# Performance work log

Measured on AMD Instinct MI355X. Metric: run time of the kernel, lower is better.

The kernel has to match this reference:

```python
import jax, jax.numpy as jnp
import numpy as np

A = 3                      # anchors per location
HS = [256, 128, 64, 32]    # square feature-map sizes (FPN levels)
B = 4                      # batch (num images)
SIZES = [A * h * h for h in HS]
T = sum(SIZES)             # 261120 anchors per image
PRE_N, POST_N = 512, 512
NMS_TH, SCORE_TH, MIN_SIZE = 0.7, 0.0, 1e-3
LOG_MAX = 4.135166556742356   # log(1000/16), standard delta clamp
MAXV = 8                      # max vertices of quad-quad intersection
LVL_OFF = 8192.0              # per-level coordinate offset for batched NMS


def box_corners(b):
    # b: [..., 5] (cx, cy, w, h, angle) -> [..., 4, 2] CCW corners
    cx, cy, w, h, a = (b[..., i] for i in range(5))
    c, s = jnp.cos(a), jnp.sin(a)
    dx = 0.5 * jnp.stack([w, -w, -w, w], -1)
    dy = 0.5 * jnp.stack([h, h, -h, -h], -1)
    x = cx[..., None] + dx * c[..., None] - dy * s[..., None]
    y = cy[..., None] + dx * s[..., None] + dy * c[..., None]
    return jnp.stack([x, y], -1)


def _clip(poly, cnt, p1, p2):
    # Sutherland-Hodgman clip of poly (padded [MAXV,2], cnt valid) by half-plane left of p1->p2
    e = p2 - p1
    d = e[0] * (poly[:, 1] - p1[1]) - e[1] * (poly[:, 0] - p1[0])
    def body(carry, i):
        out, oc = carry
        nxt = jnp.where(i + 1 < cnt, i + 1, 0)
        cur_in, nxt_in = d[i] >= 0, d[nxt] >= 0
        valid = i < cnt
        keep = valid & cur_in
        out = out.at[oc].set(jnp.where(keep, poly[i], out[oc]))
        oc = oc + keep.astype(jnp.int32)
        crs = valid & (cur_in != nxt_in)
        den = d[i] - d[nxt]
        t = d[i] / jnp.where(den == 0, 1.0, den)
        ip = poly[i] + t * (poly[nxt] - poly[i])
        out = out.at[oc].set(jnp.where(crs, ip, out[oc]))
        oc = oc + crs.astype(jnp.int32)
        return (out, oc), None
    (out, oc), _ = jax.lax.scan(body, (jnp.zeros((MAXV, 2), poly.dtype), jnp.int32(0)), jnp.arange(MAXV))
    return out, oc


def _inter_area(ca, cb):
    # intersection area of two convex quads given CCW corners [4,2]
    poly = jnp.zeros((MAXV, 2), ca.dtype).at[:4].set(ca)
    cnt = jnp.int32(4)
    for k in range(4):
        poly, cnt = _clip(poly, cnt, cb[k], cb[(k + 1) % 4])
    i = jnp.arange(MAXV)
    nxt = jnp.where(i + 1 < cnt, i + 1, 0)
    cr = poly[i, 0] * poly[nxt, 1] - poly[nxt, 0] * poly[i, 1]
    area = 0.5 * jnp.abs(jnp.sum(jnp.where(i < cnt, cr, 0.0)))
    return jnp.where(cnt >= 3, area, 0.0)


def decode(deltas, anchors):
    # XYWHA decode with 6-dim deltas (dx,dy,dw,dh,dsin,dcos), weights all 1.0
    ax, ay, aw, ah, aa = (anchors[..., i] for i in range(5))
    dx, dy, dw, dh, ds, dc = (deltas[..., i] for i in range(6))
    dw = jnp.minimum(dw, LOG_MAX)
    dh = jnp.minimum(dh, LOG_MAX)
    return jnp.stack([ax + dx * aw, ay + dy * ah, aw * jnp.exp(dw),
                      ah * jnp.exp(dh), aa + jnp.arctan2(ds, dc)], -1)


def nms_image(boxes, scores, levels):
    # boxes [N,5], scores [N] (post-sigmoid), levels [N] int32 -> fixed-size padded outputs
    N = scores.shape[0]
    valid = (boxes[:, 2] >= MIN_SIZE) & (boxes[:, 3] >= MIN_SIZE) & (scores >= SCORE_TH)
    s = jnp.where(valid, scores, -jnp.inf)
    order = jnp.argsort(-s)
    bx, sc, vd = boxes[order], s[order], valid[order]
    off = levels[order].astype(bx.dtype) * LVL_OFF
    nb = bx.at[:, :2].add(off[:, None])          # level offset => cross-level IoU == 0
    nbg = jax.lax.stop_gradient(nb)
    corners = box_corners(nbg)                    # [N,4,2]
    areas = nbg[:, 2] * nbg[:, 3]
    CH = 128
    def chunk_fn(args):
        cc, ca = args
        def row(ci, ai):
            inter = jax.vmap(lambda cj: _inter_area(ci, cj))(corners)
            return inter / (ai + areas - inter + 1e-7)
        return jax.vmap(row)(cc, ca)
    iou = jax.lax.map(chunk_fn, (corners.reshape(N // CH, CH, 4, 2),
                                 areas.reshape(N // CH, CH))).reshape(N, N)
    idx = jnp.arange(N)
    def body(i, sup):
        keep_i = ~sup[i]
        return sup | (keep_i & (iou[i] > NMS_TH) & (idx > i))
    sup = jax.lax.fori_loop(0, N, body, ~vd)      # invalid boxes start suppressed
    kept = ~sup
    _, top_i = jax.lax.top_k(jnp.where(kept, sc, -jnp.inf), POST_N)
    ok = kept[top_i]
    return jnp.where(ok[:, None], bx[top_i], 0.0), jnp.where(ok, sc[top_i], 0.0)


def rpn_forward(objs, dlts, anchors):
    obj_f, dlt_f = [], []
    for o, d, h in zip(objs, dlts, HS):
        # permute_and_flatten: [B,A,H,W] -> [B,H*W*A]; [B,A*6,H,W] -> [B,H*W*A,6]
        obj_f.append(o.transpose(0, 2, 3, 1).reshape(B, -1))
        dlt_f.append(d.reshape(B, A, 6, h, h).transpose(0, 3, 4, 1, 2).reshape(B, -1, 6))
    objectness = jnp.concatenate(obj_f, 1)        # [B, T]
    deltas = jnp.concatenate(dlt_f, 1)            # [B, T, 6]
    proposals = decode(deltas, anchors)           # [B, T, 5]
    parts, offset = [], 0
    for sz in SIZES:                               # per-level top-k
        k = min(PRE_N, sz)
        _, ti = jax.lax.top_k(objectness[:, offset:offset + sz], k)
        parts.append(ti + offset)
        offset += sz
    top_idx = jnp.concatenate(parts, 1)           # [B, 4*PRE_N]
    levels = jnp.concatenate([jnp.full((sz,), i, jnp.int32) for i, sz in enumerate(SIZES)])
    obj_top = jnp.take_along_axis(objectness, top_idx, 1)
    prop_top = jnp.take_along_axis(proposals, top_idx[..., None], 1)
    lvl_top = levels[top_idx]
    scores = jax.nn.sigmoid(obj_top)
    return jax.vmap(nms_image)(prop_top, scores, lvl_top)


def setup_inputs() -> dict:
    key = jax.random.key(0)
    ks = jax.random.split(key, 9)
    inp = {}
    for i, h in enumerate(HS):
        inp[f"obj{i}"] = jax.random.normal(ks[i], (B, A, h, h), jnp.float32)
        inp[f"dlt{i}"] = 0.25 * jax.random.normal(ks[4 + i], (B, A * 6, h, h), jnp.float32)
    u = jax.random.uniform(ks[8], (B, T, 5), jnp.float32)
    inp["anchors"] = jnp.stack([u[..., 0] * 1024.0, u[..., 1] * 1024.0,
                                8.0 + 120.0 * u[..., 2], 8.0 + 120.0 * u[..., 3],
                                jnp.pi * (u[..., 4] - 0.5)], -1)
    return inp


def reference(obj0, obj1, obj2, obj3, dlt0, dlt1, dlt2, dlt3, anchors):
    # returns (boxes [B, POST_N, 5], scores [B, POST_N]) padded with zeros
    return rpn_forward([obj0, obj1, obj2, obj3], [dlt0, dlt1, dlt2, dlt3], anchors)
```

## Files before the change

kernel.cpp:

```cpp
#include <hip/hip_runtime.h>

typedef unsigned int u32;
typedef unsigned long long u64;
typedef unsigned char u8;

#define NB 4
#define T_ANCH 261120
#define NCAND 2048
#define KSEL 512
#define POSTN 512
#define LOG_MAXF 4.135166556742356f
#define NMS_TH 0.7f
#define LVL_OFF_F 8192.0f
#define BINS 4096
#define EQCAP 8192
#define K5_BLOCKS 2048
#define K1_BLOCKS 256

__device__ __forceinline__ u32 mono32(float f){
  u32 u = __float_as_uint(f);
  return (u & 0x80000000u) ? ~u : (u | 0x80000000u);
}
__device__ __forceinline__ int lvl_hw(int lvl){ return 65536 >> (2*lvl); }
__device__ __forceinline__ int lvl_off(int lvl){
  return (lvl>0?196608:0) + (lvl>1?49152:0) + (lvl>2?12288:0);
}
__device__ __forceinline__ void k1_map(int bx, int& b, int& lvl, int& ch){
  b = bx >> 6;
  int c = bx & 63;
  if (c < 48){ lvl = 0; ch = c; }
  else if (c < 60){ lvl = 1; ch = c - 48; }
  else if (c < 63){ lvl = 2; ch = c - 60; }
  else { lvl = 3; ch = 0; }
}

__global__ __launch_bounds__(1024) void k1_hist_thresh(
    const float* __restrict__ o0, const float* __restrict__ o1,
    const float* __restrict__ o2, const float* __restrict__ o3,
    u32* __restrict__ hist16, u32* __restrict__ done16,
    u32* __restrict__ gb0, u32* __restrict__ gcA)
{
  int b, lvl, ch;
  k1_map(blockIdx.x, b, lvl, ch);
  int bid16 = b*4 + lvl;
  int nch = (lvl==0?48 : lvl==1?12 : lvl==2?3 : 1);
  const float* ob = (lvl==0)?o0 : (lvl==1)?o1 : (lvl==2)?o2 : o3;
  int hw = lvl_hw(lvl);
  int size = 3*hw;
  int n4 = size >> 2;
  int i4 = ch*1024 + threadIdx.x;
  __shared__ u32 hist[BINS];
  __shared__ u32 coarse[64];
  __shared__ int s_last;
  for (int i = threadIdx.x; i < BINS; i += 1024) hist[i] = 0;
  __syncthreads();
  if (i4 < n4){
    float4 v = ((const float4*)(ob + (size_t)b*size))[i4];
    atomicAdd(&hist[mono32(v.x) >> 20], 1u);
    atomicAdd(&hist[mono32(v.y) >> 20], 1u);
    atomicAdd(&hist[mono32(v.z) >> 20], 1u);
    atomicAdd(&hist[mono32(v.w) >> 20], 1u);
  }
  __syncthreads();
  u32* gh = hist16 + (size_t)bid16*BINS;
  for (int i = threadIdx.x; i < BINS; i += 1024){
    u32 c = hist[i];
    if (c) atomicAdd(&gh[i], c);
  }
  __syncthreads();
  if (threadIdx.x == 0){
    __threadfence();
    u32 d = atomicAdd(&done16[bid16], 1u);
    s_last = (d == (u32)(nch - 1)) ? 1 : 0;
  }
  __syncthreads();
  if (!s_last) return;

  __threadfence();
  for (int i = threadIdx.x; i < BINS; i += 1024)
    hist[i] = __hip_atomic_load(&gh[i], __ATOMIC_RELAXED, __HIP_MEMORY_SCOPE_AGENT);
  __syncthreads();
  int t = threadIdx.x;
  if (t < 64){
    u32 s = 0;
    for (int z = 0; z < 64; ++z) s += hist[t*64 + z];
    coarse[t] = s;
  }
  __syncthreads();
  if (t == 0){
    u32 acc = 0;
    int cb = 63;
    while (acc + coarse[cb] < (u32)KSEL){ acc += coarse[cb]; --cb; }
    int z = cb*64 + 63;
    while (acc + hist[z] < (u32)KSEL){ acc += hist[z]; --z; }
    gb0[bid16] = (u32)z;
    gcA[bid16] = acc;
  }
}

__global__ __launch_bounds__(1024) void k2_classify(
    const float* __restrict__ o0, const float* __restrict__ o1,
    const float* __restrict__ o2, const float* __restrict__ o3,
    const u32* __restrict__ gb0,
    u32* __restrict__ emitcnt, u32* __restrict__ tiecnt,
    int* __restrict__ cand_j, u64* __restrict__ gtie)
{
  int b, lvl, ch;
  k1_map(blockIdx.x, b, lvl, ch);
  int bid16 = b*4 + lvl;
  const float* ob = (lvl==0)?o0 : (lvl==1)?o1 : (lvl==2)?o2 : o3;
  int hw = lvl_hw(lvl);
  int size = 3*hw;
  int n4 = size >> 2;
  int i4 = ch*1024 + threadIdx.x;

  __shared__ u32 dbuf[KSEL];
  __shared__ u64 tbuf[4096];
  __shared__ u32 dn, tn, dbase, tbase;
  if (threadIdx.x == 0){ dn = 0; tn = 0; }
  __syncthreads();

  u32 b0v = gb0[bid16];
  if (i4 < n4){
    float4 v = ((const float4*)(ob + (size_t)b*size))[i4];
    int L = i4 << 2;
    int a = L / hw;
    int pix = L - a*hw;
    int j0 = pix*3 + a;
    float vv[4] = {v.x, v.y, v.z, v.w};
    #pragma unroll
    for (int q = 0; q < 4; ++q){
      u32 m = mono32(vv[q]);
      u32 bin = m >> 20;
      int j = j0 + 3*q;
      if (bin > b0v){
        u32 s = atomicAdd(&dn, 1u);
        if (s < (u32)KSEL) dbuf[s] = (u32)j;
      } else if (bin == b0v){
        u32 s = atomicAdd(&tn, 1u);
        if (s < 4096u) tbuf[s] = ((u64)m << 32) | (u32)(~(u32)j);
      }
    }
  }
  __syncthreads();
  if (threadIdx.x == 0){
    dbase = dn ? atomicAdd(&emitcnt[bid16], dn) : 0u;
    tbase = tn ? atomicAdd(&tiecnt[bid16], tn) : 0u;
  }
  __syncthreads();
  for (u32 x = threadIdx.x; x < dn; x += 1024){
    u32 s = dbase + x;
    if (s < (u32)KSEL) cand_j[bid16*KSEL + s] = (int)dbuf[x];
  }
  for (u32 x = threadIdx.x; x < tn; x += 1024){
    u32 s = tbase + x;
    if (s < (u32)EQCAP) gtie[(size_t)bid16*EQCAP + s] = tbuf[x];
  }
}

__global__ __launch_bounds__(512) void k3_tie_decode(
    const u64* __restrict__ gtie, const u32* __restrict__ tiecnt,
    const u32* __restrict__ gcA, const int* __restrict__ cand_j,
    const float* __restrict__ o0, const float* __restrict__ o1,
    const float* __restrict__ o2, const float* __restrict__ o3,
    const float* __restrict__ d0, const float* __restrict__ d1,
    const float* __restrict__ d2, const float* __restrict__ d3,
    const float* __restrict__ anchors,
    float* __restrict__ cscore, u32* __restrict__ csmono,
    u64* __restrict__ ctb, float* __restrict__ cbox, u8* __restrict__ cvalid)
{
  int bid = blockIdx.x;
  int t = threadIdx.x;
  __shared__ u64 eq[EQCAP];
  __shared__ u32 wbuf[KSEL];
  __shared__ int jlist[KSEL];
  __shared__ u32 wn;
  u32 n = tiecnt[bid]; if (n > (u32)EQCAP) n = (u32)EQCAP;
  u32 cA = gcA[bid];
  u32 k = (u32)KSEL - cA;
  if (t == 0) wn = 0;
  for (int i = t; i < KSEL; i += 512) jlist[i] = 0;
  for (u32 i = t; i < n; i += 512) eq[i] = gtie[(size_t)bid*EQCAP + i];
  __syncthreads();
  for (u32 i = t; i < n; i += 512){
    u64 ki = eq[i];
    u32 r = 0;
    for (u32 m = 0; m < n; ++m) r += (eq[m] > ki) ? 1u : 0u;
    if (r < k){
      u32 s = atomicAdd(&wn, 1u);
      if (s < (u32)KSEL) wbuf[s] = (u32)(~(u32)ki);
    }
  }
  __syncthreads();
  u32 w = wn;
  for (u32 i = t; i < cA; i += 512)
    if (i < (u32)KSEL) jlist[i] = cand_j[bid*KSEL + i];
  for (u32 x = t; x < w; x += 512){
    u32 s = cA + x;
    if (s < (u32)KSEL) jlist[s] = (int)wbuf[x];
  }
  __syncthreads();

  {
    int c = bid*KSEL + t;
    int b = bid >> 2, lvl = bid & 3;
    int j = jlist[t];
    int hw = lvl_hw(lvl);
    u32 pix = (u32)j / 3u;
    u32 a = (u32)j - pix*3u;
    const float* ob = (lvl==0)?o0 : (lvl==1)?o1 : (lvl==2)?o2 : o3;
    const float* dl = (lvl==0)?d0 : (lvl==1)?d1 : (lvl==2)?d2 : d3;

    float ov = ob[(size_t)(b*3 + (int)a)*hw + pix];
    size_t dbase = ((size_t)(b*3 + (int)a)*6)*(size_t)hw + pix;
    float dx  = dl[dbase + 0*(size_t)hw];
    float dy  = dl[dbase + 1*(size_t)hw];
    float dw  = dl[dbase + 2*(size_t)hw];
    float dh  = dl[dbase + 3*(size_t)hw];
    float dsn = dl[dbase + 4*(size_t)hw];
    float dcs = dl[dbase + 5*(size_t)hw];
    int tt = lvl_off(lvl) + j;
    const float* an = anchors + ((size_t)b*T_ANCH + tt)*5;
    float ax=an[0], ay=an[1], aw=an[2], ah=an[3], aa=an[4];
    dw = fminf(dw, LOG_MAXF); dh = fminf(dh, LOG_MAXF);
    float cx = ax + dx*aw;
    float cy = ay + dy*ah;
    float ww = aw * expf(dw);
    float hh = ah * expf(dh);
    float ang = aa + atan2f(dsn, dcs);
    double sd = 1.0 / (1.0 + exp(-(double)ov));
    float sc = (float)sd;
    bool valid = (ww >= 1e-3f) && (hh >= 1e-3f) && (sc >= 0.0f);
    cscore[c] = sc;
    csmono[c] = valid ? mono32(sc) : 0u;
    ctb[c] = ((u64)lvl << 50) | ((u64)(u32)(~mono32(ov)) << 18) | (u64)(u32)j;
    cvalid[c] = valid ? 1 : 0;
    float* bb = cbox + (size_t)c*5;
    bb[0]=cx; bb[1]=cy; bb[2]=ww; bb[3]=hh; bb[4]=ang;
  }
}

__global__ __launch_bounds__(256) void k4_rank(
    const u32* __restrict__ csmono, const u64* __restrict__ ctb,
    const float* __restrict__ cscore, const float* __restrict__ cbox,
    const u8* __restrict__ cvalid,
    float* __restrict__ sscore, float* __restrict__ sbox,
    float* __restrict__ geom, float4* __restrict__ aabb4,
    u8* __restrict__ svalid, u64* __restrict__ maskz, u64* __restrict__ rowflagz)
{
  int b   = blockIdx.x >> 6;
  int blk = blockIdx.x & 63;
  __shared__ u32 sm[NCAND];
  __shared__ u64 stb[NCAND];
  __shared__ u32 cnt[32][8];
  {
    u64* mz = maskz + (size_t)blockIdx.x * 1024;
    for (int x = threadIdx.x; x < 1024; x += 256) mz[x] = 0ull;
    if (threadIdx.x == 0 && blockIdx.x < NB*32) rowflagz[blockIdx.x] = 0ull;
  }
  for (int k = threadIdx.x; k < NCAND; k += 256){
    sm[k]  = csmono[b*NCAND + k];
    stb[k] = ctb[b*NCAND + k];
  }
  __syncthreads();
  int esub = threadIdx.x >> 3;
  int ssub = threadIdx.x & 7;
  int id = blk*32 + esub;
  u32 ms = sm[id];
  u64 mt = stb[id];
  u32 r = 0;
  #pragma unroll 8
  for (int it = 0; it < 256; ++it){
    int m = it*8 + ssub;
    u32 s2 = sm[m]; u64 t2 = stb[m];
    r += ((s2 > ms) || (s2 == ms && t2 < mt)) ? 1u : 0u;
  }
  cnt[esub][ssub] = r;
  __syncthreads();
  if (ssub == 0){
    u32 rank = 0;
    #pragma unroll
    for (int q = 0; q < 8; ++q) rank += cnt[esub][q];
    int gsrc = b*NCAND + id;
    int gdst = b*NCAND + (int)rank;
    sscore[gdst] = cscore[gsrc];
    svalid[gdst] = cvalid[gsrc];
    float b0 = cbox[(size_t)gsrc*5+0], b1 = cbox[(size_t)gsrc*5+1];
    float b2 = cbox[(size_t)gsrc*5+2], b3 = cbox[(size_t)gsrc*5+3];
    float b4 = cbox[(size_t)gsrc*5+4];
    float* sb = sbox + (size_t)gdst*5;
    sb[0]=b0; sb[1]=b1; sb[2]=b2; sb[3]=b3; sb[4]=b4;
    int lvl = (int)((mt >> 50) & 3ull);
    float offv = (float)lvl * LVL_OFF_F;
    float cx = b0 + offv, cy = b1 + offv, w=b2, h=b3, ang=b4;
    float cc = cosf(ang), sn = sinf(ang);
    float hx = 0.5f*w, hy = 0.5f*h;
    float x0 = cx + hx*cc - hy*sn, y0 = cy + hx*sn + hy*cc;
    float x1 = cx - hx*cc - hy*sn, y1 = cy - hx*sn + hy*cc;
    float x2 = cx - hx*cc + hy*sn, y2 = cy - hx*sn - hy*cc;
    float x3 = cx + hx*cc + hy*sn, y3 = cy + hx*sn - hy*cc;
    float minx = fminf(fminf(x0,x1),fminf(x2,x3));
    float maxx = fmaxf(fmaxf(x0,x1),fmaxf(x2,x3));
    float miny = fminf(fminf(y0,y1),fminf(y2,y3));
    float maxy = fmaxf(fmaxf(y0,y1),fmaxf(y2,y3));
    float* g = geom + (size_t)gdst*16;
    g[0]=minx; g[1]=maxx; g[2]=miny; g[3]=maxy; g[4]=w*h;
    g[5]=x0; g[6]=y0; g[7]=x1; g[8]=y1; g[9]=x2; g[10]=y2; g[11]=x3; g[12]=y3;
    aabb4[gdst] = make_float4(minx, maxx, miny, maxy);
  }
}

__device__ __forceinline__ void emit_pt(float* ox, float* oy, int oc, float x, float y){
  #pragma unroll
  for (int s = 0; s < 8; ++s) if (s == oc){ ox[s] = x; oy[s] = y; }
}

__device__ float quad_inter(const float* ca, const float* cb){
  float px[8], py[8];
  #pragma unroll
  for (int q = 0; q < 8; ++q){ px[q]=0.f; py[q]=0.f; }
  #pragma unroll
  for (int q = 0; q < 4; ++q){ px[q]=ca[2*q]; py[q]=ca[2*q+1]; }
  int cnt = 4;
  #pragma unroll
  for (int e = 0; e < 4; ++e){
    float p1x = cb[2*e],         p1y = cb[2*e+1];
    float p2x = cb[(2*e+2)&7],   p2y = cb[(2*e+3)&7];
    float ex = p2x-p1x, ey = p2y-p1y;
    float d[8];
    #pragma unroll
    for (int q = 0; q < 8; ++q) d[q] = ex*(py[q]-p1y) - ey*(px[q]-p1x);
    float ox[8], oy[8];
    #pragma unroll
    for (int q = 0; q < 8; ++q){ ox[q]=0.f; oy[q]=0.f; }
    int oc = 0;
    #pragma unroll
    for (int q = 0; q < 8; ++q){
      if (q < cnt){
        bool last = (q+1 >= cnt);
        float dn  = last ? d[0]  : d[(q+1)&7];
        bool in0 = (d[q] >= 0.0f), in1 = (dn >= 0.0f);
        if (in0){ emit_pt(ox,oy,oc,px[q],py[q]); oc++; }
        if (in0 != in1){
          float pnx = last ? px[0] : px[(q+1)&7];
          float pny = last ? py[0] : py[(q+1)&7];
          float den = d[q] - dn;
          float t = d[q] / ((den == 0.0f) ? 1.0f : den);
          emit_pt(ox,oy,oc, px[q] + t*(pnx-px[q]), py[q] + t*(pny-py[q]));
          oc++;
        }
      }
    }
    cnt = (oc > 8) ? 8 : oc;
    #pragma unroll
    for (int q = 0; q < 8; ++q){ px[q]=ox[q]; py[q]=oy[q]; }
  }
  if (cnt < 3) return 0.0f;
  float s = 0.0f;
  #pragma unroll
  for (int q = 0; q < 8; ++q){
    if (q < cnt){
      bool last = (q+1 >= cnt);
      float pnx = last ? px[0] : px[(q+1)&7];
      float pny = last ? py[0] : py[(q+1)&7];
      s += px[q]*pny - pnx*py[q];
    }
  }
  return 0.5f*fabsf(s);
}

__global__ __launch_bounds__(256) void k5_pairs(
    const float4* __restrict__ aabb4, const float* __restrict__ geom,
    u64* __restrict__ mask, u64* __restrict__ rowflag)
{
  __shared__ u32 lbuf[4096];
  __shared__ u32 lcnt;
  if (threadIdx.x == 0) lcnt = 0;
  __syncthreads();
  int img = blockIdx.x >> 9;
  int kk  = blockIdx.x & 511;
  int lane = threadIdx.x & 63;
  int rows[4] = {2*kk, 2*kk + 1, 2046 - 2*kk, 2047 - 2*kk};
  #pragma unroll
  for (int r = 0; r < 4; ++r){
    int i = rows[r];
    float4 gi = aabb4[img*NCAND + i];
    for (int j = i + 1 + (int)threadIdx.x; j < NCAND; j += 256){
      float4 gj = aabb4[img*NCAND + j];
      bool pass = !(gi.x > gj.y || gj.x > gi.y || gi.z > gj.w || gj.z > gi.w);
      u64 bm = __ballot(pass);
      if (bm){
        int leader = __ffsll((long long)bm) - 1;
        u32 base = 0;
        if (lane == leader) base = atomicAdd(&lcnt, (u32)__popcll(bm));
        base = (u32)__shfl((int)base, leader);
        if (pass){
          u32 off = (u32)__popcll(bm & ((1ull << lane) - 1ull));
          lbuf[base + off] = (u32)((i << 11) | j);
        }
      }
    }
  }
  __syncthreads();
  u32 n = lcnt;
  for (u32 x = threadIdx.x; x < n; x += 256){
    u32 gt = lbuf[x];
    int i = (int)(gt >> 11);
    int j = (int)(gt & (NCAND-1));
    const float* gi = geom + ((size_t)(img*NCAND + i))*16;
    const float* gj = geom + ((size_t)(img*NCAND + j))*16;
    float inter = quad_inter(gi+5, gj+5);
    float iou = inter / (gi[4] + gj[4] - inter + 1e-7f);
    if (iou > NMS_TH){
      atomicOr(&mask[((size_t)(img*NCAND + i))*32 + (j >> 6)], 1ull << (j & 63));
      atomicOr(&rowflag[(size_t)img*32 + (i >> 6)], 1ull << (i & 63));
    }
  }
}

__global__ __launch_bounds__(1024) void k6_nms_out(
    const u64* __restrict__ mask, const u64* __restrict__ rowflag,
    const u8* __restrict__ svalid,
    const float* __restrict__ sbox, const float* __restrict__ sscore,
    float* __restrict__ out)
{
  int b = blockIdx.x;
  __shared__ u32 fid[NCAND];
  __shared__ u32 wcnt[32], wpref[32];
  __shared__ u64 s_kept[32];
  __shared__ u32 pref[32];
  __shared__ u32 s_F;
  int t = threadIdx.x;
  int wid = t >> 6, lane = t & 63;

  if (t < 32) wcnt[t] = (u32)__popcll(rowflag[b*32 + t]);
  __syncthreads();
  if (t == 0){
    u32 run = 0;
    for (int w = 0; w < 32; ++w){ wpref[w] = run; run += wcnt[w]; }
    s_F = run;
  }
  __syncthreads();
  if (t < 32){
    u64 fw = rowflag[b*32 + t];
    u32 o = wpref[t];
    while (fw){
      int bpos = __builtin_ctzll(fw);
      fid[o++] = (u32)(t*64 + bpos);
      fw &= fw - 1;
    }
  }
  for (int x = t; x < POSTN*5; x += 1024) out[(size_t)b*POSTN*5 + x] = 0.0f;
  for (int x = t; x < POSTN;   x += 1024) out[(size_t)NB*POSTN*5 + b*POSTN + x] = 0.0f;
  __syncthreads();

  if (wid == 0){
    u32 slo = 0, shi = 0;
    {
      int wl = lane & 31;
      u64 w = 0;
      for (int q = 0; q < 64; ++q)
        if (!svalid[b*NCAND + wl*64 + q]) w |= (1ull << q);
      slo = (u32)w; shi = (u32)(w >> 32);
    }
    u32 F = s_F;
    const u64* mb = mask + ((size_t)b*NCAND)*32;
    for (u32 f = 0; f < F; f += 8){
      u32 myfid = 0;
      if (f + (lane & 7) < F) myfid = fid[f + (lane & 7)];
      u64 v[8];
      #pragma unroll
      for (int q = 0; q < 8; ++q){
        if (f + q < F){
          u32 fq = (u32)__builtin_amdgcn_readlane((int)myfid, q);
          v[q] = mb[(size_t)fq*32 + (lane & 31)];
        } else v[q] = 0ull;
      }
      #pragma unroll
      for (int q = 0; q < 8; ++q){
        if (f + q < F){
          u32 i = (u32)__builtin_amdgcn_readlane((int)myfid, q);
          int wi = (int)(i >> 6);
          u32 wlo = (u32)__builtin_amdgcn_readlane((int)slo, wi);
          u32 whi = (u32)__builtin_amdgcn_readlane((int)shi, wi);
          u64 w = ((u64)whi << 32) | wlo;
          u32 keep = (u32)((~w >> (i & 63)) & 1ull);
          u64 vm = v[q] & (0ull - (u64)keep);
          slo |= (u32)vm; shi |= (u32)(vm >> 32);
        }
      }
    }
    if (lane < 32) s_kept[lane] = ~(((u64)shi << 32) | slo);
  }
  __syncthreads();

  if (t < 32) pref[t] = (u32)__popcll(s_kept[t]);
  __syncthreads();
  if (t == 0){
    u32 run = 0;
    for (int w = 0; w < 32; ++w){ u32 tv = pref[w]; pref[w] = run; run += tv; }
  }
  __syncthreads();
  for (int i = t; i < NCAND; i += 1024){
    u64 kw = s_kept[i >> 6];
    if ((kw >> (i & 63)) & 1ull){
      u32 rank = pref[i >> 6] + (u32)__popcll(kw & ((1ull << (i & 63)) - 1ull));
      if (rank < POSTN){
        const float* bp = sbox + ((size_t)(b*NCAND + i))*5;
        float* op = out + ((size_t)(b*POSTN + rank))*5;
        op[0]=bp[0]; op[1]=bp[1]; op[2]=bp[2]; op[3]=bp[3]; op[4]=bp[4];
        out[(size_t)NB*POSTN*5 + b*POSTN + rank] = sscore[b*NCAND + i];
      }
    }
  }
}

extern "C" void kernel_launch(void* const* d_in, const int* in_sizes, int n_in,
                              void* d_out, int out_size, void* d_ws, size_t ws_size,
                              hipStream_t stream)
{
  (void)out_size; (void)ws_size;
  const float *obj[4] = {nullptr,nullptr,nullptr,nullptr};
  const float *dlt[4] = {nullptr,nullptr,nullptr,nullptr};
  const float *anchors = nullptr;
  for (int i = 0; i < n_in; ++i){
    int s = in_sizes[i];
    const float* p = (const float*)d_in[i];
    switch (s){
      case 786432:  obj[0] = p; break;
      case 4718592: dlt[0] = p; break;
      case 196608:  obj[1] = p; break;
      case 1179648: dlt[1] = p; break;
      case 49152:   obj[2] = p; break;
      case 294912:  dlt[2] = p; break;
      case 12288:   obj[3] = p; break;
      case 73728:   dlt[3] = p; break;
      case 5222400: anchors = p; break;
      default: break;
    }
  }

  char* wsb = (char*)d_ws;
  size_t off = 0;
  auto alloc = [&](size_t bytes)->void*{
    size_t cur = (off + 255) & ~(size_t)255;
    off = cur + bytes;
    return (void*)(wsb + cur);
  };
  int*   cand_j = (int*)  alloc(16*KSEL*sizeof(int));
  float* cscore = (float*)alloc((size_t)NB*NCAND*sizeof(float));
  u32*   csmono = (u32*)  alloc((size_t)NB*NCAND*sizeof(u32));
  u64*   ctb    = (u64*)  alloc((size_t)NB*NCAND*sizeof(u64));
  float* cbox   = (float*)alloc((size_t)NB*NCAND*5*sizeof(float));
  u8*    cvalid = (u8*)   alloc((size_t)NB*NCAND);
  float* sscore = (float*)alloc((size_t)NB*NCAND*sizeof(float));
  float* sbox   = (float*)alloc((size_t)NB*NCAND*5*sizeof(float));
  u8*    svalid = (u8*)   alloc((size_t)NB*NCAND);
  float* geom   = (float*)alloc((size_t)NB*NCAND*16*sizeof(float));
  float4* aabb4 = (float4*)alloc((size_t)NB*NCAND*sizeof(float4));
  u64*   gtie   = (u64*)  alloc((size_t)16*EQCAP*sizeof(u64));
  u64*   maskp  = (u64*)  alloc((size_t)NB*NCAND*32*sizeof(u64));
  u64*   rowflag= (u64*)  alloc((size_t)NB*32*sizeof(u64));
  u32*   gb0    = (u32*)  alloc(16*sizeof(u32));
  u32*   gcA    = (u32*)  alloc(16*sizeof(u32));
  u32*   hist16 = (u32*)  alloc((size_t)16*BINS*sizeof(u32));
  u32*   done16 = (u32*)  alloc(16*sizeof(u32));
  u32*   emitc  = (u32*)  alloc(16*sizeof(u32));
  u32*   tiec   = (u32*)  alloc(16*sizeof(u32));
  size_t zero_len = (size_t)((wsb + off) - (char*)hist16);

  hipMemsetAsync(hist16, 0, zero_len, stream);

  hipLaunchKernelGGL(k1_hist_thresh, dim3(K1_BLOCKS), dim3(1024), 0, stream,
                     obj[0], obj[1], obj[2], obj[3], hist16, done16, gb0, gcA);
  hipLaunchKernelGGL(k2_classify, dim3(K1_BLOCKS), dim3(1024), 0, stream,
                     obj[0], obj[1], obj[2], obj[3], gb0, emitc, tiec,
                     cand_j, gtie);
  hipLaunchKernelGGL(k3_tie_decode, dim3(16), dim3(512), 0, stream,
                     gtie, tiec, gcA, cand_j,
                     obj[0], obj[1], obj[2], obj[3],
                     dlt[0], dlt[1], dlt[2], dlt[3],
                     anchors, cscore, csmono, ctb, cbox, cvalid);
  hipLaunchKernelGGL(k4_rank, dim3(256), dim3(256), 0, stream,
                     csmono, ctb, cscore, cbox, cvalid, sscore, sbox, geom,
                     aabb4, svalid, maskp, rowflag);
  hipLaunchKernelGGL(k5_pairs, dim3(K5_BLOCKS), dim3(256), 0, stream,
                     aabb4, geom, maskp, rowflag);
  hipLaunchKernelGGL(k6_nms_out, dim3(4), dim3(1024), 0, stream,
                     maskp, rowflag, svalid, sbox, sscore, (float*)d_out);
}
```

Before: 192.3 us.

## Fuse top-k kernels and pair/NMS-output kernels using grid-wide completion counters

Merges the histogram-threshold, classify and tie-decode kernels into one launch. Non-last blocks spin-wait on a published flag for the per-level threshold, and the last block to finish classification does the tie resolution and decode. Likewise, the pair-overlap kernel and the final NMS/output kernel are fused, so the last block per image runs the greedy suppression. This removes launch gaps and the re-read of objectness. The spin-wait relies on all 256 blocks of 1024 threads being co-resident, and the serial tail runs on only one block per group.

```diff
diff --git a/kernel.cpp b/kernel.cpp
--- a/kernel.cpp
+++ b/kernel.cpp
@@ -34,183 +34,191 @@
   else { lvl = 3; ch = 0; }
 }
 
-__global__ __launch_bounds__(1024) void k1_hist_thresh(
-    const float* __restrict__ o0, const float* __restrict__ o1,
-    const float* __restrict__ o2, const float* __restrict__ o3,
-    u32* __restrict__ hist16, u32* __restrict__ done16,
-    u32* __restrict__ gb0, u32* __restrict__ gcA)
-{
-  int b, lvl, ch;
-  k1_map(blockIdx.x, b, lvl, ch);
-  int bid16 = b*4 + lvl;
-  int nch = (lvl==0?48 : lvl==1?12 : lvl==2?3 : 1);
-  const float* ob = (lvl==0)?o0 : (lvl==1)?o1 : (lvl==2)?o2 : o3;
-  int hw = lvl_hw(lvl);
-  int size = 3*hw;
-  int n4 = size >> 2;
-  int i4 = ch*1024 + threadIdx.x;
-  __shared__ u32 hist[BINS];
-  __shared__ u32 coarse[64];
-  __shared__ int s_last;
-  for (int i = threadIdx.x; i < BINS; i += 1024) hist[i] = 0;
-  __syncthreads();
-  if (i4 < n4){
-    float4 v = ((const float4*)(ob + (size_t)b*size))[i4];
-    atomicAdd(&hist[mono32(v.x) >> 20], 1u);
-    atomicAdd(&hist[mono32(v.y) >> 20], 1u);
-    atomicAdd(&hist[mono32(v.z) >> 20], 1u);
-    atomicAdd(&hist[mono32(v.w) >> 20], 1u);
-  }
-  __syncthreads();
-  u32* gh = hist16 + (size_t)bid16*BINS;
-  for (int i = threadIdx.x; i < BINS; i += 1024){
-    u32 c = hist[i];
-    if (c) atomicAdd(&gh[i], c);
-  }
-  __syncthreads();
-  if (threadIdx.x == 0){
-    __threadfence();
-    u32 d = atomicAdd(&done16[bid16], 1u);
-    s_last = (d == (u32)(nch - 1)) ? 1 : 0;
-  }
-  __syncthreads();
-  if (!s_last) return;
-
-  __threadfence();
-  for (int i = threadIdx.x; i < BINS; i += 1024)
-    hist[i] = __hip_atomic_load(&gh[i], __ATOMIC_RELAXED, __HIP_MEMORY_SCOPE_AGENT);
-  __syncthreads();
-  int t = threadIdx.x;
-  if (t < 64){
-    u32 s = 0;
-    for (int z = 0; z < 64; ++z) s += hist[t*64 + z];
-    coarse[t] = s;
-  }
-  __syncthreads();
-  if (t == 0){
-    u32 acc = 0;
-    int cb = 63;
-    while (acc + coarse[cb] < (u32)KSEL){ acc += coarse[cb]; --cb; }
-    int z = cb*64 + 63;
-    while (acc + hist[z] < (u32)KSEL){ acc += hist[z]; --z; }
-    gb0[bid16] = (u32)z;
-    gcA[bid16] = acc;
-  }
-}
-
-__global__ __launch_bounds__(1024) void k2_classify(
-    const float* __restrict__ o0, const float* __restrict__ o1,
-    const float* __restrict__ o2, const float* __restrict__ o3,
-    const u32* __restrict__ gb0,
-    u32* __restrict__ emitcnt, u32* __restrict__ tiecnt,
-    int* __restrict__ cand_j, u64* __restrict__ gtie)
-{
-  int b, lvl, ch;
-  k1_map(blockIdx.x, b, lvl, ch);
-  int bid16 = b*4 + lvl;
-  const float* ob = (lvl==0)?o0 : (lvl==1)?o1 : (lvl==2)?o2 : o3;
-  int hw = lvl_hw(lvl);
-  int size = 3*hw;
-  int n4 = size >> 2;
-  int i4 = ch*1024 + threadIdx.x;
-
-  __shared__ u32 dbuf[KSEL];
-  __shared__ u64 tbuf[4096];
-  __shared__ u32 dn, tn, dbase, tbase;
-  if (threadIdx.x == 0){ dn = 0; tn = 0; }
-  __syncthreads();
-
-  u32 b0v = gb0[bid16];
-  if (i4 < n4){
-    float4 v = ((const float4*)(ob + (size_t)b*size))[i4];
-    int L = i4 << 2;
-    int a = L / hw;
-    int pix = L - a*hw;
-    int j0 = pix*3 + a;
-    float vv[4] = {v.x, v.y, v.z, v.w};
-    #pragma unroll
-    for (int q = 0; q < 4; ++q){
-      u32 m = mono32(vv[q]);
-      u32 bin = m >> 20;
-      int j = j0 + 3*q;
-      if (bin > b0v){
-        u32 s = atomicAdd(&dn, 1u);
-        if (s < (u32)KSEL) dbuf[s] = (u32)j;
-      } else if (bin == b0v){
-        u32 s = atomicAdd(&tn, 1u);
-        if (s < 4096u) tbuf[s] = ((u64)m << 32) | (u32)(~(u32)j);
-      }
-    }
-  }
-  __syncthreads();
-  if (threadIdx.x == 0){
-    dbase = dn ? atomicAdd(&emitcnt[bid16], dn) : 0u;
-    tbase = tn ? atomicAdd(&tiecnt[bid16], tn) : 0u;
-  }
-  __syncthreads();
-  for (u32 x = threadIdx.x; x < dn; x += 1024){
-    u32 s = dbase + x;
-    if (s < (u32)KSEL) cand_j[bid16*KSEL + s] = (int)dbuf[x];
-  }
-  for (u32 x = threadIdx.x; x < tn; x += 1024){
-    u32 s = tbase + x;
-    if (s < (u32)EQCAP) gtie[(size_t)bid16*EQCAP + s] = tbuf[x];
-  }
-}
-
-__global__ __launch_bounds__(512) void k3_tie_decode(
-    const u64* __restrict__ gtie, const u32* __restrict__ tiecnt,
-    const u32* __restrict__ gcA, const int* __restrict__ cand_j,
+union ShA {
+  struct { u32 hist[BINS]; u32 coarse[64]; } a;
+  struct { u32 dbuf[KSEL]; u64 tbuf[4096]; } c;
+  struct { u64 eq[EQCAP]; u32 wbuf[KSEL]; int jlist[KSEL]; } p3;
+};
+
+__global__ __launch_bounds__(1024) void k123(
     const float* __restrict__ o0, const float* __restrict__ o1,
     const float* __restrict__ o2, const float* __restrict__ o3,
     const float* __restrict__ d0, const float* __restrict__ d1,
     const float* __restrict__ d2, const float* __restrict__ d3,
     const float* __restrict__ anchors,
+    u32* __restrict__ hist16, u32* __restrict__ done16,
+    u32* __restrict__ pub16, u32* __restrict__ cls_done,
+    u32* __restrict__ gb0, u32* __restrict__ gcA,
+    u32* __restrict__ emitc, u32* __restrict__ tiec,
+    int* __restrict__ cand_j, u64* __restrict__ gtie,
     float* __restrict__ cscore, u32* __restrict__ csmono,
     u64* __restrict__ ctb, float* __restrict__ cbox, u8* __restrict__ cvalid)
 {
-  int bid = blockIdx.x;
-  int t = threadIdx.x;
-  __shared__ u64 eq[EQCAP];
-  __shared__ u32 wbuf[KSEL];
-  __shared__ int jlist[KSEL];
-  __shared__ u32 wn;
-  u32 n = tiecnt[bid]; if (n > (u32)EQCAP) n = (u32)EQCAP;
-  u32 cA = gcA[bid];
+  __shared__ ShA sh;
+  __shared__ int s_last, s_last2;
+  __shared__ u32 s_b0, s_cA, s_dn, s_tn, s_dbase, s_tbase, s_wn;
+  const int t = threadIdx.x;
+  int b, lvl, ch;
+  k1_map(blockIdx.x, b, lvl, ch);
+  const int bid16 = b*4 + lvl;
+  const int nch = (lvl==0?48 : lvl==1?12 : lvl==2?3 : 1);
+  const float* ob = (lvl==0)?o0 : (lvl==1)?o1 : (lvl==2)?o2 : o3;
+  const int hw = lvl_hw(lvl);
+  const int size = 3*hw;
+  const int n4 = size >> 2;
+  const int i4 = ch*1024 + t;
+  const bool has = (i4 < n4);
+
+  u32 m0=0,m1=0,m2=0,m3=0;
+  int j0 = 0;
+  if (has){
+    float4 v = ((const float4*)(ob + (size_t)b*size))[i4];
+    m0 = mono32(v.x); m1 = mono32(v.y); m2 = mono32(v.z); m3 = mono32(v.w);
+    int L = i4 << 2;
+    int a = L / hw;
+    int pix = L - a*hw;
+    j0 = pix*3 + a;
+  }
+  for (int i = t; i < BINS; i += 1024) sh.a.hist[i] = 0;
+  __syncthreads();
+  if (has){
+    atomicAdd(&sh.a.hist[m0 >> 20], 1u);
+    atomicAdd(&sh.a.hist[m1 >> 20], 1u);
+    atomicAdd(&sh.a.hist[m2 >> 20], 1u);
+    atomicAdd(&sh.a.hist[m3 >> 20], 1u);
+  }
+  __syncthreads();
+  u32* gh = hist16 + (size_t)bid16*BINS;
+  for (int i = t; i < BINS; i += 1024){
+    u32 c = sh.a.hist[i];
+    if (c) atomicAdd(&gh[i], c);
+  }
+  __syncthreads();
+  if (t == 0){
+    __threadfence();
+    u32 d = atomicAdd(&done16[bid16], 1u);
+    s_last = (d == (u32)(nch - 1)) ? 1 : 0;
+  }
+  __syncthreads();
+
+  if (s_last){
+    for (int i = t; i < BINS; i += 1024)
+      sh.a.hist[i] = __hip_atomic_load(&gh[i], __ATOMIC_RELAXED, __HIP_MEMORY_SCOPE_AGENT);
+    __syncthreads();
+    if (t < 64){
+      u32 s = 0;
+      for (int z = 0; z < 64; ++z) s += sh.a.hist[t*64 + z];
+      sh.a.coarse[t] = s;
+    }
+    __syncthreads();
+    if (t == 0){
+      u32 acc = 0;
+      int cb = 63;
+      while (acc + sh.a.coarse[cb] < (u32)KSEL){ acc += sh.a.coarse[cb]; --cb; }
+      int z = cb*64 + 63;
+      while (acc + sh.a.hist[z] < (u32)KSEL){ acc += sh.a.hist[z]; --z; }
+      s_b0 = (u32)z; s_cA = acc;
+      __hip_atomic_store(&gb0[bid16], (u32)z, __ATOMIC_RELAXED, __HIP_MEMORY_SCOPE_AGENT);
+      __hip_atomic_store(&gcA[bid16], acc,   __ATOMIC_RELAXED, __HIP_MEMORY_SCOPE_AGENT);
+      __threadfence();
+      __hip_atomic_store(&pub16[bid16], 1u, __ATOMIC_RELEASE, __HIP_MEMORY_SCOPE_AGENT);
+    }
+  } else {
+    if (t == 0){
+      while (__hip_atomic_load(&pub16[bid16], __ATOMIC_ACQUIRE, __HIP_MEMORY_SCOPE_AGENT) == 0u)
+        __builtin_amdgcn_s_sleep(2);
+      s_b0 = __hip_atomic_load(&gb0[bid16], __ATOMIC_RELAXED, __HIP_MEMORY_SCOPE_AGENT);
+      s_cA = __hip_atomic_load(&gcA[bid16], __ATOMIC_RELAXED, __HIP_MEMORY_SCOPE_AGENT);
+    }
+  }
+  __syncthreads();
+  const u32 b0v = s_b0;
+  const u32 cA  = s_cA;
+  __syncthreads();
+
+  if (t == 0){ s_dn = 0; s_tn = 0; }
+  __syncthreads();
+  if (has){
+    u32 mm[4] = {m0, m1, m2, m3};
+    #pragma unroll
+    for (int q = 0; q < 4; ++q){
+      u32 m = mm[q];
+      u32 bin = m >> 20;
+      int j = j0 + 3*q;
+      if (bin > b0v){
+        u32 s = atomicAdd(&s_dn, 1u);
+        if (s < (u32)KSEL) sh.c.dbuf[s] = (u32)j;
+      } else if (bin == b0v){
+        u32 s = atomicAdd(&s_tn, 1u);
+        if (s < 4096u) sh.c.tbuf[s] = ((u64)m << 32) | (u32)(~(u32)j);
+      }
+    }
+  }
+  __syncthreads();
+  if (t == 0){
+    s_dbase = s_dn ? atomicAdd(&emitc[bid16], s_dn) : 0u;
+    s_tbase = s_tn ? atomicAdd(&tiec[bid16], s_tn) : 0u;
+  }
+  __syncthreads();
+  for (u32 x = t; x < s_dn; x += 1024){
+    u32 s = s_dbase + x;
+    if (s < (u32)KSEL)
+      __hip_atomic_store(&cand_j[bid16*KSEL + s], (int)sh.c.dbuf[x],
+                         __ATOMIC_RELAXED, __HIP_MEMORY_SCOPE_AGENT);
+  }
+  for (u32 x = t; x < s_tn; x += 1024){
+    u32 s = s_tbase + x;
+    if (s < (u32)EQCAP)
+      __hip_atomic_store(&gtie[(size_t)bid16*EQCAP + s], sh.c.tbuf[x],
+                         __ATOMIC_RELAXED, __HIP_MEMORY_SCOPE_AGENT);
+  }
+  __syncthreads();
+  if (t == 0){
+    __threadfence();
+    u32 d = __hip_atomic_fetch_add(&cls_done[bid16], 1u,
+                                   __ATOMIC_ACQ_REL, __HIP_MEMORY_SCOPE_AGENT);
+    s_last2 = (d == (u32)(nch - 1)) ? 1 : 0;
+  }
+  __syncthreads();
+  if (!s_last2) return;
+
+  u32 n = __hip_atomic_load(&tiec[bid16], __ATOMIC_RELAXED, __HIP_MEMORY_SCOPE_AGENT);
+  if (n > (u32)EQCAP) n = (u32)EQCAP;
   u32 k = (u32)KSEL - cA;
-  if (t == 0) wn = 0;
-  for (int i = t; i < KSEL; i += 512) jlist[i] = 0;
-  for (u32 i = t; i < n; i += 512) eq[i] = gtie[(size_t)bid*EQCAP + i];
-  __syncthreads();
-  for (u32 i = t; i < n; i += 512){
-    u64 ki = eq[i];
+  if (t == 0) s_wn = 0;
+  __syncthreads();
+  for (int i = t; i < KSEL; i += 1024) sh.p3.jlist[i] = 0;
+  for (u32 i = t; i < n; i += 1024)
+    sh.p3.eq[i] = __hip_atomic_load(&gtie[(size_t)bid16*EQCAP + i],
+                                    __ATOMIC_RELAXED, __HIP_MEMORY_SCOPE_AGENT);
+  __syncthreads();
+  for (u32 i = t; i < n; i += 1024){
+    u64 ki = sh.p3.eq[i];
     u32 r = 0;
-    for (u32 m = 0; m < n; ++m) r += (eq[m] > ki) ? 1u : 0u;
+    for (u32 m = 0; m < n; ++m) r += (sh.p3.eq[m] > ki) ? 1u : 0u;
     if (r < k){
-      u32 s = atomicAdd(&wn, 1u);
-      if (s < (u32)KSEL) wbuf[s] = (u32)(~(u32)ki);
-    }
-  }
-  __syncthreads();
-  u32 w = wn;
-  for (u32 i = t; i < cA; i += 512)
-    if (i < (u32)KSEL) jlist[i] = cand_j[bid*KSEL + i];
-  for (u32 x = t; x < w; x += 512){
+      u32 s = atomicAdd(&s_wn, 1u);
+      if (s < (u32)KSEL) sh.p3.wbuf[s] = (u32)(~(u32)ki);
+    }
+  }
+  __syncthreads();
+  u32 w = s_wn; if (w > (u32)KSEL) w = (u32)KSEL;
+  for (u32 i = t; i < cA; i += 1024)
+    if (i < (u32)KSEL)
+      sh.p3.jlist[i] = __hip_atomic_load(&cand_j[bid16*KSEL + i],
+                                         __ATOMIC_RELAXED, __HIP_MEMORY_SCOPE_AGENT);
+  for (u32 x = t; x < w; x += 1024){
     u32 s = cA + x;
-    if (s < (u32)KSEL) jlist[s] = (int)wbuf[x];
-  }
-  __syncthreads();
-
-  {
-    int c = bid*KSEL + t;
-    int b = bid >> 2, lvl = bid & 3;
-    int j = jlist[t];
-    int hw = lvl_hw(lvl);
+    if (s < (u32)KSEL) sh.p3.jlist[s] = (int)sh.p3.wbuf[x];
+  }
+  __syncthreads();
+
+  if (t < KSEL){
+    int c = bid16*KSEL + t;
+    int j = sh.p3.jlist[t];
     u32 pix = (u32)j / 3u;
     u32 a = (u32)j - pix*3u;
-    const float* ob = (lvl==0)?o0 : (lvl==1)?o1 : (lvl==2)?o2 : o3;
     const float* dl = (lvl==0)?d0 : (lvl==1)?d1 : (lvl==2)?d2 : d3;
-
     float ov = ob[(size_t)(b*3 + (int)a)*hw + pix];
     size_t dbase = ((size_t)(b*3 + (int)a)*6)*(size_t)hw + pix;
     float dx  = dl[dbase + 0*(size_t)hw];
@@ -369,42 +377,54 @@
   return 0.5f*fabsf(s);
 }
 
-__global__ __launch_bounds__(256) void k5_pairs(
+union Sh56 {
+  struct { u32 lbuf[4096]; } a;
+  struct { u32 fid[NCAND]; u64 rfw[32]; u32 wcnt[32], wpref[32];
+           u64 s_kept[32]; u32 pref[32]; u32 sF; } b;
+};
+
+__global__ __launch_bounds__(256) void k56_pairs_out(
     const float4* __restrict__ aabb4, const float* __restrict__ geom,
-    u64* __restrict__ mask, u64* __restrict__ rowflag)
+    u64* __restrict__ mask, u64* __restrict__ rowflag,
+    u32* __restrict__ clipdone,
+    const u8* __restrict__ svalid,
+    const float* __restrict__ sbox, const float* __restrict__ sscore,
+    float* __restrict__ out)
 {
-  __shared__ u32 lbuf[4096];
-  __shared__ u32 lcnt;
-  if (threadIdx.x == 0) lcnt = 0;
+  __shared__ Sh56 sh;
+  __shared__ u32 s_lcnt;
+  __shared__ int s_w;
+  const int t = threadIdx.x;
+  if (t == 0) s_lcnt = 0;
   __syncthreads();
   int img = blockIdx.x >> 9;
   int kk  = blockIdx.x & 511;
-  int lane = threadIdx.x & 63;
+  int lane = t & 63;
   int rows[4] = {2*kk, 2*kk + 1, 2046 - 2*kk, 2047 - 2*kk};
   #pragma unroll
   for (int r = 0; r < 4; ++r){
     int i = rows[r];
     float4 gi = aabb4[img*NCAND + i];
-    for (int j = i + 1 + (int)threadIdx.x; j < NCAND; j += 256){
+    for (int j = i + 1 + t; j < NCAND; j += 256){
       float4 gj = aabb4[img*NCAND + j];
       bool pass = !(gi.x > gj.y || gj.x > gi.y || gi.z > gj.w || gj.z > gi.w);
       u64 bm = __ballot(pass);
       if (bm){
         int leader = __ffsll((long long)bm) - 1;
         u32 base = 0;
-        if (lane == leader) base = atomicAdd(&lcnt, (u32)__popcll(bm));
+        if (lane == leader) base = atomicAdd(&s_lcnt, (u32)__popcll(bm));
         base = (u32)__shfl((int)base, leader);
         if (pass){
           u32 off = (u32)__popcll(bm & ((1ull << lane) - 1ull));
-          lbuf[base + off] = (u32)((i << 11) | j);
+          sh.a.lbuf[base + off] = (u32)((i << 11) | j);
         }
       }
     }
   }
   __syncthreads();
-  u32 n = lcnt;
-  for (u32 x = threadIdx.x; x < n; x += 256){
-    u32 gt = lbuf[x];
+  u32 n = s_lcnt;
+  for (u32 x = t; x < n; x += 256){
+    u32 gt = sh.a.lbuf[x];
     int i = (int)(gt >> 11);
     int j = (int)(gt & (NCAND-1));
     const float* gi = geom + ((size_t)(img*NCAND + i))*16;
@@ -416,45 +436,44 @@
       atomicOr(&rowflag[(size_t)img*32 + (i >> 6)], 1ull << (i & 63));
     }
   }
-}
-
-__global__ __launch_bounds__(1024) void k6_nms_out(
-    const u64* __restrict__ mask, const u64* __restrict__ rowflag,
-    const u8* __restrict__ svalid,
-    const float* __restrict__ sbox, const float* __restrict__ sscore,
-    float* __restrict__ out)
-{
-  int b = blockIdx.x;
-  __shared__ u32 fid[NCAND];
-  __shared__ u32 wcnt[32], wpref[32];
-  __shared__ u64 s_kept[32];
-  __shared__ u32 pref[32];
-  __shared__ u32 s_F;
-  int t = threadIdx.x;
-  int wid = t >> 6, lane = t & 63;
-
-  if (t < 32) wcnt[t] = (u32)__popcll(rowflag[b*32 + t]);
+  __syncthreads();
+  if (t == 0){
+    __threadfence();
+    u32 d = __hip_atomic_fetch_add(&clipdone[img], 1u,
+                                   __ATOMIC_ACQ_REL, __HIP_MEMORY_SCOPE_AGENT);
+    s_w = (d == 511u) ? 1 : 0;
+  }
+  __syncthreads();
+  if (!s_w) return;
+
+  const int b = img;
+  __syncthreads();
+  if (t < 32)
+    sh.b.rfw[t] = __hip_atomic_load(&rowflag[b*32 + t],
+                                    __ATOMIC_RELAXED, __HIP_MEMORY_SCOPE_AGENT);
+  __syncthreads();
+  if (t < 32) sh.b.wcnt[t] = (u32)__popcll(sh.b.rfw[t]);
   __syncthreads();
   if (t == 0){
     u32 run = 0;
-    for (int w = 0; w < 32; ++w){ wpref[w] = run; run += wcnt[w]; }
-    s_F = run;
+    for (int w = 0; w < 32; ++w){ sh.b.wpref[w] = run; run += sh.b.wcnt[w]; }
+    sh.b.sF = run;
   }
   __syncthreads();
   if (t < 32){
-    u64 fw = rowflag[b*32 + t];
-    u32 o = wpref[t];
+    u64 fw = sh.b.rfw[t];
+    u32 o = sh.b.wpref[t];
     while (fw){
       int bpos = __builtin_ctzll(fw);
-      fid[o++] = (u32)(t*64 + bpos);
+      sh.b.fid[o++] = (u32)(t*64 + bpos);
       fw &= fw - 1;
     }
   }
-  for (int x = t; x < POSTN*5; x += 1024) out[(size_t)b*POSTN*5 + x] = 0.0f;
-  for (int x = t; x < POSTN;   x += 1024) out[(size_t)NB*POSTN*5 + b*POSTN + x] = 0.0f;
-  __syncthreads();
-
-  if (wid == 0){
+  for (int x = t; x < POSTN*5; x += 256) out[(size_t)b*POSTN*5 + x] = 0.0f;
+  for (int x = t; x < POSTN;   x += 256) out[(size_t)NB*POSTN*5 + b*POSTN + x] = 0.0f;
+  __syncthreads();
+
+  if ((t >> 6) == 0){
     u32 slo = 0, shi = 0;
     {
       int wl = lane & 31;
@@ -463,17 +482,18 @@
         if (!svalid[b*NCAND + wl*64 + q]) w |= (1ull << q);
       slo = (u32)w; shi = (u32)(w >> 32);
     }
-    u32 F = s_F;
+    u32 F = sh.b.sF;
     const u64* mb = mask + ((size_t)b*NCAND)*32;
     for (u32 f = 0; f < F; f += 8){
       u32 myfid = 0;
-      if (f + (lane & 7) < F) myfid = fid[f + (lane & 7)];
+      if (f + (lane & 7) < F) myfid = sh.b.fid[f + (lane & 7)];
       u64 v[8];
       #pragma unroll
       for (int q = 0; q < 8; ++q){
         if (f + q < F){
           u32 fq = (u32)__builtin_amdgcn_readlane((int)myfid, q);
-          v[q] = mb[(size_t)fq*32 + (lane & 31)];
+          v[q] = __hip_atomic_load(&mb[(size_t)fq*32 + (lane & 31)],
+                                   __ATOMIC_RELAXED, __HIP_MEMORY_SCOPE_AGENT);
         } else v[q] = 0ull;
       }
       #pragma unroll
@@ -490,21 +510,21 @@
         }
       }
     }
-    if (lane < 32) s_kept[lane] = ~(((u64)shi << 32) | slo);
-  }
-  __syncthreads();
-
-  if (t < 32) pref[t] = (u32)__popcll(s_kept[t]);
+    if (lane < 32) sh.b.s_kept[lane] = ~(((u64)shi << 32) | slo);
+  }
+  __syncthreads();
+
+  if (t < 32) sh.b.pref[t] = (u32)__popcll(sh.b.s_kept[t]);
   __syncthreads();
   if (t == 0){
     u32 run = 0;
-    for (int w = 0; w < 32; ++w){ u32 tv = pref[w]; pref[w] = run; run += tv; }
-  }
-  __syncthreads();
-  for (int i = t; i < NCAND; i += 1024){
-    u64 kw = s_kept[i >> 6];
+    for (int w = 0; w < 32; ++w){ u32 tv = sh.b.pref[w]; sh.b.pref[w] = run; run += tv; }
+  }
+  __syncthreads();
+  for (int i = t; i < NCAND; i += 256){
+    u64 kw = sh.b.s_kept[i >> 6];
     if ((kw >> (i & 63)) & 1ull){
-      u32 rank = pref[i >> 6] + (u32)__popcll(kw & ((1ull << (i & 63)) - 1ull));
+      u32 rank = sh.b.pref[i >> 6] + (u32)__popcll(kw & ((1ull << (i & 63)) - 1ull));
       if (rank < POSTN){
         const float* bp = sbox + ((size_t)(b*NCAND + i))*5;
         float* op = out + ((size_t)(b*POSTN + rank))*5;
@@ -565,27 +585,24 @@
   u32*   gcA    = (u32*)  alloc(16*sizeof(u32));
   u32*   hist16 = (u32*)  alloc((size_t)16*BINS*sizeof(u32));
   u32*   done16 = (u32*)  alloc(16*sizeof(u32));
+  u32*   pub16  = (u32*)  alloc(16*sizeof(u32));
+  u32*   clsdn  = (u32*)  alloc(16*sizeof(u32));
+  u32*   clipdn = (u32*)  alloc(NB*sizeof(u32));
   u32*   emitc  = (u32*)  alloc(16*sizeof(u32));
   u32*   tiec   = (u32*)  alloc(16*sizeof(u32));
   size_t zero_len = (size_t)((wsb + off) - (char*)hist16);
 
   hipMemsetAsync(hist16, 0, zero_len, stream);
 
-  hipLaunchKernelGGL(k1_hist_thresh, dim3(K1_BLOCKS), dim3(1024), 0, stream,
-                     obj[0], obj[1], obj[2], obj[3], hist16, done16, gb0, gcA);
-  hipLaunchKernelGGL(k2_classify, dim3(K1_BLOCKS), dim3(1024), 0, stream,
-                     obj[0], obj[1], obj[2], obj[3], gb0, emitc, tiec,
-                     cand_j, gtie);
-  hipLaunchKernelGGL(k3_tie_decode, dim3(16), dim3(512), 0, stream,
-                     gtie, tiec, gcA, cand_j,
+  hipLaunchKernelGGL(k123, dim3(K1_BLOCKS), dim3(1024), 0, stream,
                      obj[0], obj[1], obj[2], obj[3],
-                     dlt[0], dlt[1], dlt[2], dlt[3],
-                     anchors, cscore, csmono, ctb, cbox, cvalid);
+                     dlt[0], dlt[1], dlt[2], dlt[3], anchors,
+                     hist16, done16, pub16, clsdn, gb0, gcA, emitc, tiec,
+                     cand_j, gtie, cscore, csmono, ctb, cbox, cvalid);
   hipLaunchKernelGGL(k4_rank, dim3(256), dim3(256), 0, stream,
                      csmono, ctb, cscore, cbox, cvalid, sscore, sbox, geom,
                      aabb4, svalid, maskp, rowflag);
-  hipLaunchKernelGGL(k5_pairs, dim3(K5_BLOCKS), dim3(256), 0, stream,
-                     aabb4, geom, maskp, rowflag);
-  hipLaunchKernelGGL(k6_nms_out, dim3(4), dim3(1024), 0, stream,
-                     maskp, rowflag, svalid, sbox, sscore, (float*)d_out);
-}
+  hipLaunchKernelGGL(k56_pairs_out, dim3(K5_BLOCKS), dim3(256), 0, stream,
+                     aabb4, geom, maskp, rowflag, clipdn,
+                     svalid, sbox, sscore, (float*)d_out);
+}
```

Result: slower. 270.9 us (+40.9%).

## Restrict NMS pair tests to same-level candidates and prefilter by AABB IoU bound

Applied to the files above, without the earlier changes.

k4_rank now buckets the sorted candidates by FPN level into per-image, per-level index lists. k5_pairs then tests only pairs within a level, since the 8192 per-level offset means boxes on different levels cannot overlap. Each block stages that level's AABBs and areas in shared memory, and before the exact polygon clip it drops pairs whose AABB-overlap IoU upper bound cannot exceed the threshold. This cuts the O(N^2) AABB scan and the number of quad_inter calls. It relies on each level holding exactly KSEL (512) candidates, and the lvlidx capacity check silently drops any extras.

```diff
diff --git a/kernel.cpp b/kernel.cpp
--- a/kernel.cpp
+++ b/kernel.cpp
@@ -246,7 +246,8 @@
     const u8* __restrict__ cvalid,
     float* __restrict__ sscore, float* __restrict__ sbox,
     float* __restrict__ geom, float4* __restrict__ aabb4,
-    u8* __restrict__ svalid, u64* __restrict__ maskz, u64* __restrict__ rowflagz)
+    u8* __restrict__ svalid, u64* __restrict__ maskz, u64* __restrict__ rowflagz,
+    u32* __restrict__ lvlcnt, u32* __restrict__ lvlidx)
 {
   int b   = blockIdx.x >> 6;
   int blk = blockIdx.x & 63;
@@ -291,6 +292,8 @@
     float* sb = sbox + (size_t)gdst*5;
     sb[0]=b0; sb[1]=b1; sb[2]=b2; sb[3]=b3; sb[4]=b4;
     int lvl = (int)((mt >> 50) & 3ull);
+    u32 pos = atomicAdd(&lvlcnt[b*4 + lvl], 1u);
+    if (pos < (u32)KSEL) lvlidx[(u32)(b*4 + lvl)*KSEL + pos] = (u32)rank;
     float offv = (float)lvl * LVL_OFF_F;
     float cx = b0 + offv, cy = b1 + offv, w=b2, h=b3, ang=b4;
     float cc = cosf(ang), sn = sinf(ang);
@@ -370,49 +373,73 @@
 }
 
 __global__ __launch_bounds__(256) void k5_pairs(
+    const u32* __restrict__ lvlidx,
     const float4* __restrict__ aabb4, const float* __restrict__ geom,
     u64* __restrict__ mask, u64* __restrict__ rowflag)
 {
-  __shared__ u32 lbuf[4096];
+  __shared__ u32   s_idx[KSEL];
+  __shared__ float4 s_ab[KSEL];
+  __shared__ float  s_ar[KSEL];
+  __shared__ u32   lbuf[1024];
   __shared__ u32 lcnt;
-  if (threadIdx.x == 0) lcnt = 0;
-  __syncthreads();
+  const int t = threadIdx.x;
+  if (t == 0) lcnt = 0;
   int img = blockIdx.x >> 9;
-  int kk  = blockIdx.x & 511;
-  int lane = threadIdx.x & 63;
-  int rows[4] = {2*kk, 2*kk + 1, 2046 - 2*kk, 2047 - 2*kk};
+  int r9  = blockIdx.x & 511;
+  int lvl = r9 >> 7;
+  int kk  = r9 & 127;
+  int lane = t & 63;
+  const int base = (img*4 + lvl)*KSEL;
+  for (int q = t; q < KSEL; q += 256){
+    u32 rk = lvlidx[base + q];
+    s_idx[q] = rk;
+    s_ab[q]  = aabb4[img*NCAND + rk];
+    s_ar[q]  = geom[((size_t)(img*NCAND + rk))*16 + 4];
+  }
+  __syncthreads();
+  int rows[4] = {2*kk, 2*kk + 1, 510 - 2*kk, 511 - 2*kk};
   #pragma unroll
   for (int r = 0; r < 4; ++r){
-    int i = rows[r];
-    float4 gi = aabb4[img*NCAND + i];
-    for (int j = i + 1 + (int)threadIdx.x; j < NCAND; j += 256){
-      float4 gj = aabb4[img*NCAND + j];
-      bool pass = !(gi.x > gj.y || gj.x > gi.y || gi.z > gj.w || gj.z > gi.w);
+    int p = rows[r];
+    float4 gi = s_ab[p];
+    float  ai = s_ar[p];
+    for (int q = p + 1 + t; q < KSEL; q += 256){
+      float4 gj = s_ab[q];
+      float w = fminf(gi.y, gj.y) - fmaxf(gi.x, gj.x);
+      float h = fminf(gi.w, gj.w) - fmaxf(gi.z, gj.z);
+      bool pass = (w > 0.0f) && (h > 0.0f);
+      if (pass){
+        float iA = w*h;
+        float S  = ai + s_ar[q];
+        pass = ((1.0f + NMS_TH)*iA >= NMS_TH*S*(1.0f - 1e-5f));
+      }
       u64 bm = __ballot(pass);
       if (bm){
         int leader = __ffsll((long long)bm) - 1;
-        u32 base = 0;
-        if (lane == leader) base = atomicAdd(&lcnt, (u32)__popcll(bm));
-        base = (u32)__shfl((int)base, leader);
+        u32 bs = 0;
+        if (lane == leader) bs = atomicAdd(&lcnt, (u32)__popcll(bm));
+        bs = (u32)__shfl((int)bs, leader);
         if (pass){
           u32 off = (u32)__popcll(bm & ((1ull << lane) - 1ull));
-          lbuf[base + off] = (u32)((i << 11) | j);
+          lbuf[bs + off] = (u32)((p << 9) | q);
         }
       }
     }
   }
   __syncthreads();
   u32 n = lcnt;
-  for (u32 x = threadIdx.x; x < n; x += 256){
-    u32 gt = lbuf[x];
-    int i = (int)(gt >> 11);
-    int j = (int)(gt & (NCAND-1));
-    const float* gi = geom + ((size_t)(img*NCAND + i))*16;
-    const float* gj = geom + ((size_t)(img*NCAND + j))*16;
+  for (u32 x = t; x < n; x += 256){
+    u32 pr = lbuf[x];
+    int p = (int)(pr >> 9), q = (int)(pr & 511);
+    u32 ri = s_idx[p], rj = s_idx[q];
+    u32 i = ri < rj ? ri : rj;
+    u32 j = ri < rj ? rj : ri;
+    const float* gi = geom + ((size_t)(img*NCAND + (int)i))*16;
+    const float* gj = geom + ((size_t)(img*NCAND + (int)j))*16;
     float inter = quad_inter(gi+5, gj+5);
     float iou = inter / (gi[4] + gj[4] - inter + 1e-7f);
     if (iou > NMS_TH){
-      atomicOr(&mask[((size_t)(img*NCAND + i))*32 + (j >> 6)], 1ull << (j & 63));
+      atomicOr(&mask[((size_t)(img*NCAND + (int)i))*32 + (j >> 6)], 1ull << (j & 63));
       atomicOr(&rowflag[(size_t)img*32 + (i >> 6)], 1ull << (i & 63));
     }
   }
@@ -561,12 +588,14 @@
   u64*   gtie   = (u64*)  alloc((size_t)16*EQCAP*sizeof(u64));
   u64*   maskp  = (u64*)  alloc((size_t)NB*NCAND*32*sizeof(u64));
   u64*   rowflag= (u64*)  alloc((size_t)NB*32*sizeof(u64));
+  u32*   lvlidx = (u32*)  alloc((size_t)16*KSEL*sizeof(u32));
   u32*   gb0    = (u32*)  alloc(16*sizeof(u32));
   u32*   gcA    = (u32*)  alloc(16*sizeof(u32));
   u32*   hist16 = (u32*)  alloc((size_t)16*BINS*sizeof(u32));
   u32*   done16 = (u32*)  alloc(16*sizeof(u32));
   u32*   emitc  = (u32*)  alloc(16*sizeof(u32));
   u32*   tiec   = (u32*)  alloc(16*sizeof(u32));
+  u32*   lvlcnt = (u32*)  alloc(16*sizeof(u32));
   size_t zero_len = (size_t)((wsb + off) - (char*)hist16);
 
   hipMemsetAsync(hist16, 0, zero_len, stream);
@@ -583,9 +612,9 @@
                      anchors, cscore, csmono, ctb, cbox, cvalid);
   hipLaunchKernelGGL(k4_rank, dim3(256), dim3(256), 0, stream,
                      csmono, ctb, cscore, cbox, cvalid, sscore, sbox, geom,
-                     aabb4, svalid, maskp, rowflag);
+                     aabb4, svalid, maskp, rowflag, lvlcnt, lvlidx);
   hipLaunchKernelGGL(k5_pairs, dim3(K5_BLOCKS), dim3(256), 0, stream,
-                     aabb4, geom, maskp, rowflag);
+                     lvlidx, aabb4, geom, maskp, rowflag);
   hipLaunchKernelGGL(k6_nms_out, dim3(4), dim3(1024), 0, stream,
                      maskp, rowflag, svalid, sbox, sscore, (float*)d_out);
 }
```

Measured after the change: 271.2 us. 1.41x slower.
